# Optimization experiments

Measured on AMD Instinct MI355X. Metric: run time of the kernel, lower is better.

## Reference

```python
import jax, jax.numpy as jnp
import numpy as np
from jax import lax

R, D = 600, 240          # n_rna, n_dis
N = R + D                # graph nodes
H, C = 8, 64             # heads, per-head out channels
E = 20000                # edges
NEG_SLOPE = 0.2
F_CNN = 6 * (64 + 61 + 49 + 33)  # 1242 = concat of four conv branches


def setup_inputs():
    key = jax.random.key(0)
    ks = jax.random.split(key, 25)
    g = lambda i, shape, s=0.1: (jax.random.normal(ks[i], shape, jnp.float32) * s)
    return {
        'edge_index': jax.random.randint(ks[0], (2, E), 0, N, jnp.int32),
        'met_feature': jax.random.normal(ks[1], (R, R), jnp.float32),
        'dis_feature': jax.random.normal(ks[2], (D, D), jnp.float32),
        'rel_matrix': (jax.random.uniform(ks[3], (R, D)) < 0.1).astype(jnp.float32),
        'W_rna': g(4, (R, C)), 'W_dis': g(5, (D, C)),
        'W_l': g(6, (C, H * C)), 'b_l': jnp.zeros((H * C,), jnp.float32),
        'W_r': g(7, (C, H * C)), 'b_r': jnp.zeros((H * C,), jnp.float32),
        'att': g(8, (H, C)), 'gat_bias': jnp.zeros((H * C,), jnp.float32),
        'conv1_w': g(9, (6, 1, H, 1)), 'conv1_b': jnp.zeros((6,), jnp.float32),
        'conv4_w': g(10, (6, 1, H, 4)), 'conv4_b': jnp.zeros((6,), jnp.float32),
        'conv16_w': g(11, (6, 1, H, 16)), 'conv16_b': jnp.zeros((6,), jnp.float32),
        'conv32_w': g(12, (6, 1, H, 32)), 'conv32_b': jnp.zeros((6,), jnp.float32),
        'W_fc': g(13, (F_CNN, F_CNN), 0.02), 'b_fc': jnp.zeros((F_CNN,), jnp.float32),
    }


def gatv2(x, edge_index, W_l, b_l, W_r, b_r, att, bias):
    """GATv2Conv with concat=True and self-loops (eval mode, no dropout)."""
    loop = jnp.arange(N, dtype=edge_index.dtype)
    src = jnp.concatenate([edge_index[0], loop])
    dst = jnp.concatenate([edge_index[1], loop])
    xl = (x @ W_l + b_l).reshape(N, H, C)   # source transform
    xr = (x @ W_r + b_r).reshape(N, H, C)   # target transform
    e = jax.nn.leaky_relu(xl[src] + xr[dst], NEG_SLOPE)      # [Etot,H,C]
    logits = jnp.einsum('ehc,hc->eh', e, att)                 # [Etot,H]
    m = jax.ops.segment_max(logits, dst, num_segments=N)      # [N,H]
    ex = jnp.exp(logits - m[dst])
    denom = jax.ops.segment_sum(ex, dst, num_segments=N)
    alpha = ex / (denom[dst] + 1e-16)                         # edge softmax per dst
    out = jax.ops.segment_sum(alpha[:, :, None] * xl[src], dst, num_segments=N)
    return out.reshape(N, H * C) + bias


def conv_branch(x, w, b):
    # x: [N,1,H,C], w: [6,1,H,k] -> valid conv collapses head dim -> [N,6,1,C-k+1]
    y = lax.conv_general_dilated(x, w, (1, 1), 'VALID',
                                 dimension_numbers=('NCHW', 'OIHW', 'NCHW'))
    y = jax.nn.relu(y + b[None, :, None, None])
    return y.reshape(y.shape[0], -1)


def reference(edge_index, met_feature, dis_feature, rel_matrix, W_rna, W_dis,
              W_l, b_l, W_r, b_r, att, gat_bias,
              conv1_w, conv1_b, conv4_w, conv4_b, conv16_w, conv16_b,
              conv32_w, conv32_b, W_fc, b_fc):
    met_f = met_feature @ W_rna                 # [R,C]
    dis_f = dis_feature @ W_dis                 # [D,C]
    h = jnp.concatenate([met_f, dis_f], axis=0)  # [N,C]
    res = gatv2(h, edge_index, W_l, b_l, W_r, b_r, att, gat_bias)  # [N,H*C]
    x = res.reshape(N, 1, H, C)
    cat = jnp.concatenate([
        conv_branch(x, conv1_w, conv1_b),
        conv_branch(x, conv4_w, conv4_b),
        conv_branch(x, conv16_w, conv16_b),
        conv_branch(x, conv32_w, conv32_b)], axis=1)             # [N,F_CNN]
    feat = jax.nn.relu(cat @ W_fc + b_fc)                        # FeatureTransform
    rna, dis = feat[:R], feat[R:]
    # vectorized replacement of the python double loop: pairwise elementwise product
    pairs = (rna[:, None, :] * dis[None, :, :]).reshape(R * D, F_CNN)
    labels = rel_matrix.reshape(-1, 1)
    return (pairs, labels)
```

## Files before the change

### kernel.cpp

```cpp
#include <hip/hip_runtime.h>
#include <hip/hip_bf16.h>

#define R_ 600
#define D_ 240
#define N_ 840
#define H_ 8
#define C_ 64
#define HC_ 512
#define E_ 20000
#define NE_ 20840
#define F_ 1242
#define PAIRS_ 144000
#define NEG_SLOPE 0.2f

#define OFF_H     0
#define OFF_XL    53760
#define OFF_XR    483840
#define OFF_LOG   913920
#define OFF_MKEY  1080640
#define OFF_DEN   1087360
#define OFF_RES   1094080
#define OFF_CAT   1524160
#define OFF_FEAT  2567440
#define WS_END    3610720
#define ZERO_OFF  OFF_MKEY
#define ZERO_CNT  (6720 + 6720 + 430080)

__device__ __forceinline__ unsigned fkey(float x) {
    unsigned u = __float_as_uint(x);
    return (u & 0x80000000u) ? ~u : (u | 0x80000000u);
}
__device__ __forceinline__ float funkey(unsigned k) {
    unsigned u = (k & 0x80000000u) ? (k ^ 0x80000000u) : ~k;
    return __uint_as_float(u);
}

__global__ void k_zero(float* ws) {
    int i = blockIdx.x * 256 + threadIdx.x;
    if (i < ZERO_CNT) ws[ZERO_OFF + i] = 0.0f;
}

__global__ void k_h(const float* __restrict__ met, const float* __restrict__ dis,
                    const float* __restrict__ Wr,  const float* __restrict__ Wd,
                    float* __restrict__ ws) {
    __shared__ float row_s[R_];
    int n = blockIdx.x, c = threadIdx.x;
    const float *src, *W; int K;
    if (n < R_) { src = met + (size_t)n * R_; W = Wr; K = R_; }
    else        { src = dis + (size_t)(n - R_) * D_; W = Wd; K = D_; }
    for (int k = c; k < K; k += 64) row_s[k] = src[k];
    __syncthreads();
    float acc = 0.f;
    for (int k = 0; k < K; ++k) acc = fmaf(row_s[k], W[k * C_ + c], acc);
    ws[OFF_H + n * C_ + c] = acc;
}

__global__ void k_xlr(const float* __restrict__ Wl, const float* __restrict__ bl,
                      const float* __restrict__ Wr, const float* __restrict__ br,
                      float* __restrict__ ws) {
    __shared__ float hs[C_];
    int n = blockIdx.x, j = threadIdx.x;
    if (j < C_) hs[j] = ws[OFF_H + n * C_ + j];
    __syncthreads();
    float al = bl[j], ar = br[j];
    #pragma unroll
    for (int k = 0; k < C_; ++k) {
        float hv = hs[k];
        al = fmaf(hv, Wl[k * HC_ + j], al);
        ar = fmaf(hv, Wr[k * HC_ + j], ar);
    }
    ws[OFF_XL + n * HC_ + j] = al;
    ws[OFF_XR + n * HC_ + j] = ar;
}

__global__ void k_logits(const int* __restrict__ ei, const float* __restrict__ att,
                         float* __restrict__ ws) {
    int wave = blockIdx.x * 4 + (threadIdx.x >> 6);
    int lane = threadIdx.x & 63;
    if (wave >= NE_) return;
    int e = wave, src, dst;
    if (e < E_) { src = ei[e]; dst = ei[E_ + e]; }
    else        { src = dst = e - E_; }
    const float* xls = ws + OFF_XL + (size_t)src * HC_;
    const float* xrs = ws + OFF_XR + (size_t)dst * HC_;
    unsigned* mkey = (unsigned*)(ws + OFF_MKEY);
    #pragma unroll
    for (int hh = 0; hh < H_; ++hh) {
        float v = xls[hh * C_ + lane] + xrs[hh * C_ + lane];
        v = v > 0.f ? v : NEG_SLOPE * v;
        float p = att[hh * C_ + lane] * v;
        #pragma unroll
        for (int o = 32; o; o >>= 1) p += __shfl_xor(p, o, 64);
        if (lane == 0) {
            ws[OFF_LOG + e * H_ + hh] = p;
            atomicMax(&mkey[dst * H_ + hh], fkey(p));
        }
    }
}

__global__ void k_accum(const int* __restrict__ ei, float* __restrict__ ws) {
    int wave = blockIdx.x * 4 + (threadIdx.x >> 6);
    int lane = threadIdx.x & 63;
    if (wave >= NE_) return;
    int e = wave, src, dst;
    if (e < E_) { src = ei[e]; dst = ei[E_ + e]; }
    else        { src = dst = e - E_; }
    const float* xls = ws + OFF_XL + (size_t)src * HC_;
    const unsigned* mkey = (const unsigned*)(ws + OFF_MKEY);
    float* den = ws + OFF_DEN;
    float* res = ws + OFF_RES + (size_t)dst * HC_;
    #pragma unroll
    for (int hh = 0; hh < H_; ++hh) {
        float lg = ws[OFF_LOG + e * H_ + hh];
        float m  = funkey(mkey[dst * H_ + hh]);
        float ex = expf(lg - m);
        if (lane == 0) atomicAdd(&den[dst * H_ + hh], ex);
        atomicAdd(&res[hh * C_ + lane], ex * xls[hh * C_ + lane]);
    }
}

__global__ void k_conv(const float* __restrict__ gbias,
                       const float* __restrict__ c1w, const float* __restrict__ c1b,
                       const float* __restrict__ c4w, const float* __restrict__ c4b,
                       const float* __restrict__ c16w, const float* __restrict__ c16b,
                       const float* __restrict__ c32w, const float* __restrict__ c32b,
                       float* __restrict__ ws) {
    __shared__ float xsh[HC_];
    __shared__ float wsh[2544];
    __shared__ float cbs[24];
    int n = blockIdx.x, t = threadIdx.x;
    for (int i = t; i < 48;   i += 256) wsh[i]        = c1w[i];
    for (int i = t; i < 192;  i += 256) wsh[48 + i]   = c4w[i];
    for (int i = t; i < 768;  i += 256) wsh[240 + i]  = c16w[i];
    for (int i = t; i < 1536; i += 256) wsh[1008 + i] = c32w[i];
    if (t < 6) { cbs[t] = c1b[t]; cbs[6 + t] = c4b[t]; cbs[12 + t] = c16b[t]; cbs[18 + t] = c32b[t]; }
    for (int i = t; i < HC_; i += 256) {
        int hh = i >> 6;
        float d = ws[OFF_DEN + n * H_ + hh] + 1e-16f;
        xsh[i] = ws[OFF_RES + (size_t)n * HC_ + i] / d + gbias[i];
    }
    __syncthreads();
    for (int f = t; f < F_; f += 256) {
        int k, o, w, wof; float bias;
        if (f < 384)       { k = 1;  o = f / 64;  w = f - o * 64;              wof = 0;    bias = cbs[o]; }
        else if (f < 750)  { k = 4;  int f2 = f - 384;  o = f2 / 61; w = f2 - o * 61; wof = 48;   bias = cbs[6 + o]; }
        else if (f < 1044) { k = 16; int f2 = f - 750;  o = f2 / 49; w = f2 - o * 49; wof = 240;  bias = cbs[12 + o]; }
        else               { k = 32; int f2 = f - 1044; o = f2 / 33; w = f2 - o * 33; wof = 1008; bias = cbs[18 + o]; }
        float acc = bias;
        const float* wp = &wsh[wof + o * H_ * k];
        for (int hh = 0; hh < H_; ++hh)
            for (int dw = 0; dw < k; ++dw)
                acc = fmaf(xsh[hh * C_ + w + dw], wp[hh * k + dw], acc);
        ws[OFF_CAT + (size_t)n * F_ + f] = acc > 0.f ? acc : 0.f;
    }
}

#define BM 64
#define BN 64
#define BK 32
__global__ __launch_bounds__(256) void k_fc(const float* __restrict__ Wfc,
                                            const float* __restrict__ bfc,
                                            float* __restrict__ ws) {
    __shared__ float As[BK][BM + 4];
    __shared__ float Bs[BK][BN];
    const float* A = ws + OFF_CAT;
    float* Cc = ws + OFF_FEAT;
    int bm = blockIdx.y * BM, bn = blockIdx.x * BN;
    int t = threadIdx.x, tx = t & 15, ty = t >> 4;
    float acc[4][4] = {};
    for (int k0 = 0; k0 < F_; k0 += BK) {
        #pragma unroll
        for (int q = 0; q < 8; ++q) {
            int idx = q * 256 + t;
            int ml = idx >> 5, kl = idx & 31;
            int gm = bm + ml, gk = k0 + kl;
            As[kl][ml] = (gm < N_ && gk < F_) ? A[(size_t)gm * F_ + gk] : 0.f;
            int kb = idx >> 6, nb = idx & 63;
            int gkb = k0 + kb, gn = bn + nb;
            Bs[kb][nb] = (gkb < F_ && gn < F_) ? Wfc[(size_t)gkb * F_ + gn] : 0.f;
        }
        __syncthreads();
        #pragma unroll
        for (int kk = 0; kk < BK; ++kk) {
            float a[4], b[4];
            #pragma unroll
            for (int i = 0; i < 4; ++i) a[i] = As[kk][ty * 4 + i];
            #pragma unroll
            for (int j = 0; j < 4; ++j) b[j] = Bs[kk][tx * 4 + j];
            #pragma unroll
            for (int i = 0; i < 4; ++i)
                #pragma unroll
                for (int j = 0; j < 4; ++j)
                    acc[i][j] = fmaf(a[i], b[j], acc[i][j]);
        }
        __syncthreads();
    }
    #pragma unroll
    for (int i = 0; i < 4; ++i) {
        int gm = bm + ty * 4 + i;
        if (gm >= N_) break;
        #pragma unroll
        for (int j = 0; j < 4; ++j) {
            int gn = bn + tx * 4 + j;
            if (gn < F_) {
                float v = acc[i][j] + bfc[gn];
                Cc[(size_t)gm * F_ + gn] = v > 0.f ? v : 0.f;
            }
        }
    }
}

#define PPB 32
__global__ __launch_bounds__(256) void k_pairs(const float* __restrict__ ws, float* __restrict__ out) {
    int t = threadIdx.x;
    for (int pp = 0; pp < PPB; ++pp) {
        int p = blockIdx.x * PPB + pp;
        int i = p / D_, j = p - i * D_;
        const float2* rr = (const float2*)(ws + OFF_FEAT + (size_t)i * F_);
        const float2* dd = (const float2*)(ws + OFF_FEAT + (size_t)(R_ + j) * F_);
        float2* oo = (float2*)(out + (size_t)p * F_);
        for (int x = t; x < F_ / 2; x += 256) {
            float2 a = rr[x], b = dd[x];
            oo[x] = make_float2(a.x * b.x, a.y * b.y);
        }
    }
}

__global__ void k_labels(const float* __restrict__ rel, float* __restrict__ out) {
    int i = blockIdx.x * 256 + threadIdx.x;
    if (i < PAIRS_) out[(size_t)PAIRS_ * F_ + i] = rel[i];
}

extern "C" void kernel_launch(void* const* d_in, const int* in_sizes, int n_in,
                              void* d_out, int out_size, void* d_ws, size_t ws_size,
                              hipStream_t stream) {
    const int*   ei   = (const int*)  d_in[0];
    const float* met  = (const float*)d_in[1];
    const float* dis  = (const float*)d_in[2];
    const float* rel  = (const float*)d_in[3];
    const float* Wrna = (const float*)d_in[4];
    const float* Wdis = (const float*)d_in[5];
    const float* Wl   = (const float*)d_in[6];
    const float* bl   = (const float*)d_in[7];
    const float* Wr   = (const float*)d_in[8];
    const float* br   = (const float*)d_in[9];
    const float* att  = (const float*)d_in[10];
    const float* gb   = (const float*)d_in[11];
    const float* c1w  = (const float*)d_in[12];
    const float* c1b  = (const float*)d_in[13];
    const float* c4w  = (const float*)d_in[14];
    const float* c4b  = (const float*)d_in[15];
    const float* c16w = (const float*)d_in[16];
    const float* c16b = (const float*)d_in[17];
    const float* c32w = (const float*)d_in[18];
    const float* c32b = (const float*)d_in[19];
    const float* Wfc  = (const float*)d_in[20];
    const float* bfc  = (const float*)d_in[21];
    float* ws  = (float*)d_ws;
    float* out = (float*)d_out;

    hipLaunchKernelGGL(k_zero,   dim3((ZERO_CNT + 255) / 256), dim3(256), 0, stream, ws);
    hipLaunchKernelGGL(k_h,      dim3(N_),   dim3(64),  0, stream, met, dis, Wrna, Wdis, ws);
    hipLaunchKernelGGL(k_xlr,    dim3(N_),   dim3(512), 0, stream, Wl, bl, Wr, br, ws);
    hipLaunchKernelGGL(k_logits, dim3((NE_ + 3) / 4), dim3(256), 0, stream, ei, att, ws);
    hipLaunchKernelGGL(k_accum,  dim3((NE_ + 3) / 4), dim3(256), 0, stream, ei, ws);
    hipLaunchKernelGGL(k_conv,   dim3(N_),   dim3(256), 0, stream,
                       gb, c1w, c1b, c4w, c4b, c16w, c16b, c32w, c32b, ws);
    hipLaunchKernelGGL(k_fc,     dim3((F_ + BN - 1) / BN, (N_ + BM - 1) / BM), dim3(256), 0, stream, Wfc, bfc, ws);
    hipLaunchKernelGGL(k_pairs,  dim3(PAIRS_ / PPB), dim3(256), 0, stream, ws, out);
    hipLaunchKernelGGL(k_labels, dim3((PAIRS_ + 255) / 256), dim3(256), 0, stream, rel, out);
}
```

Before: 1.248 ms.

## Replace atomic edge-scatter GATv2 with CSR-by-destination per-node softmax aggregation

Builds a CSR grouping of edges by destination using a histogram, a single-block scan and a scatter. One block per destination node then computes logits, the softmax and the weighted sum without float atomics, and applies normalization and bias before writing. This removes the atomicMax/atomicAdd traffic on the result rows and the logits buffer. The FC GEMM tile height is halved to launch more blocks. It relies on a fixed MAXDEG of 256 shared-memory slots per node, so higher in-degree would overflow, and it adds three small launches.

```diff
diff --git a/kernel.cpp b/kernel.cpp
--- a/kernel.cpp
+++ b/kernel.cpp
@@ -12,32 +12,23 @@
 #define F_ 1242
 #define PAIRS_ 144000
 #define NEG_SLOPE 0.2f
+#define MAXDEG 256
 
 #define OFF_H     0
 #define OFF_XL    53760
 #define OFF_XR    483840
-#define OFF_LOG   913920
-#define OFF_MKEY  1080640
-#define OFF_DEN   1087360
-#define OFF_RES   1094080
-#define OFF_CAT   1524160
-#define OFF_FEAT  2567440
-#define WS_END    3610720
-#define ZERO_OFF  OFF_MKEY
-#define ZERO_CNT  (6720 + 6720 + 430080)
-
-__device__ __forceinline__ unsigned fkey(float x) {
-    unsigned u = __float_as_uint(x);
-    return (u & 0x80000000u) ? ~u : (u | 0x80000000u);
-}
-__device__ __forceinline__ float funkey(unsigned k) {
-    unsigned u = (k & 0x80000000u) ? (k ^ 0x80000000u) : ~k;
-    return __uint_as_float(u);
-}
+#define OFF_RES   913920
+#define OFF_CAT   1344000
+#define OFF_FEAT  2387280
+#define OFF_DEG   3430560
+#define OFF_OFFS  3431400
+#define OFF_POS   3432241
+#define OFF_ESRC  3433081
+#define WS_END    3453921
 
 __global__ void k_zero(float* ws) {
     int i = blockIdx.x * 256 + threadIdx.x;
-    if (i < ZERO_CNT) ws[ZERO_OFF + i] = 0.0f;
+    if (i < N_) ((int*)(ws + OFF_DEG))[i] = 0;
 }
 
 __global__ void k_h(const float* __restrict__ met, const float* __restrict__ dis,
@@ -73,54 +64,100 @@
     ws[OFF_XR + n * HC_ + j] = ar;
 }
 
-__global__ void k_logits(const int* __restrict__ ei, const float* __restrict__ att,
-                         float* __restrict__ ws) {
-    int wave = blockIdx.x * 4 + (threadIdx.x >> 6);
-    int lane = threadIdx.x & 63;
-    if (wave >= NE_) return;
-    int e = wave, src, dst;
+__global__ void k_hist(const int* __restrict__ ei, float* __restrict__ ws) {
+    int e = blockIdx.x * 256 + threadIdx.x;
+    if (e >= NE_) return;
+    int dst = (e < E_) ? ei[E_ + e] : e - E_;
+    atomicAdd((int*)(ws + OFF_DEG) + dst, 1);
+}
+
+__global__ __launch_bounds__(1024) void k_scan(float* __restrict__ ws) {
+    __shared__ int sa[1024], sb[1024];
+    int t = threadIdx.x;
+    const int* deg = (const int*)(ws + OFF_DEG);
+    int* offs = (int*)(ws + OFF_OFFS);
+    int* pos  = (int*)(ws + OFF_POS);
+    int d = (t < N_) ? deg[t] : 0;
+    sa[t] = d;
+    __syncthreads();
+    int *cur = sa, *nxt = sb;
+    for (int off = 1; off < 1024; off <<= 1) {
+        int v = cur[t] + (t >= off ? cur[t - off] : 0);
+        nxt[t] = v;
+        __syncthreads();
+        int* tmp = cur; cur = nxt; nxt = tmp;
+    }
+    if (t < N_) {
+        offs[t + 1] = cur[t];
+        pos[t] = cur[t] - d;
+    }
+    if (t == 0) offs[0] = 0;
+}
+
+__global__ void k_scatter(const int* __restrict__ ei, float* __restrict__ ws) {
+    int e = blockIdx.x * 256 + threadIdx.x;
+    if (e >= NE_) return;
+    int src, dst;
     if (e < E_) { src = ei[e]; dst = ei[E_ + e]; }
     else        { src = dst = e - E_; }
-    const float* xls = ws + OFF_XL + (size_t)src * HC_;
-    const float* xrs = ws + OFF_XR + (size_t)dst * HC_;
-    unsigned* mkey = (unsigned*)(ws + OFF_MKEY);
-    #pragma unroll
-    for (int hh = 0; hh < H_; ++hh) {
-        float v = xls[hh * C_ + lane] + xrs[hh * C_ + lane];
-        v = v > 0.f ? v : NEG_SLOPE * v;
-        float p = att[hh * C_ + lane] * v;
-        #pragma unroll
-        for (int o = 32; o; o >>= 1) p += __shfl_xor(p, o, 64);
-        if (lane == 0) {
-            ws[OFF_LOG + e * H_ + hh] = p;
-            atomicMax(&mkey[dst * H_ + hh], fkey(p));
-        }
-    }
-}
-
-__global__ void k_accum(const int* __restrict__ ei, float* __restrict__ ws) {
-    int wave = blockIdx.x * 4 + (threadIdx.x >> 6);
-    int lane = threadIdx.x & 63;
-    if (wave >= NE_) return;
-    int e = wave, src, dst;
-    if (e < E_) { src = ei[e]; dst = ei[E_ + e]; }
-    else        { src = dst = e - E_; }
-    const float* xls = ws + OFF_XL + (size_t)src * HC_;
-    const unsigned* mkey = (const unsigned*)(ws + OFF_MKEY);
-    float* den = ws + OFF_DEN;
-    float* res = ws + OFF_RES + (size_t)dst * HC_;
-    #pragma unroll
-    for (int hh = 0; hh < H_; ++hh) {
-        float lg = ws[OFF_LOG + e * H_ + hh];
-        float m  = funkey(mkey[dst * H_ + hh]);
-        float ex = expf(lg - m);
-        if (lane == 0) atomicAdd(&den[dst * H_ + hh], ex);
-        atomicAdd(&res[hh * C_ + lane], ex * xls[hh * C_ + lane]);
-    }
-}
-
-__global__ void k_conv(const float* __restrict__ gbias,
-                       const float* __restrict__ c1w, const float* __restrict__ c1b,
+    int idx = atomicAdd((int*)(ws + OFF_POS) + dst, 1);
+    ((int*)(ws + OFF_ESRC))[idx] = src;
+}
+
+__global__ __launch_bounds__(256) void k_gat(const float* __restrict__ att,
+                                             const float* __restrict__ gbias,
+                                             float* __restrict__ ws) {
+    __shared__ int   s_src[MAXDEG];
+    __shared__ float s_w[MAXDEG][H_];
+    __shared__ float s_d[H_];
+    int dst = blockIdx.x, t = threadIdx.x;
+    const int* offs = (const int*)(ws + OFF_OFFS);
+    const int* esrc = (const int*)(ws + OFF_ESRC);
+    int beg = offs[dst], deg = offs[dst + 1] - beg;
+    for (int i = t; i < deg; i += 256) s_src[i] = esrc[beg + i];
+    __syncthreads();
+    int lane = t & 63, g = t >> 6;
+    const float* xr_row = ws + OFF_XR + (size_t)dst * HC_;
+    for (int hh = g; hh < H_; hh += 4) {
+        float a  = att[hh * C_ + lane];
+        float xr = xr_row[hh * C_ + lane];
+        for (int i = 0; i < deg; ++i) {
+            float v = ws[OFF_XL + (size_t)s_src[i] * HC_ + hh * C_ + lane] + xr;
+            v = v > 0.f ? v : NEG_SLOPE * v;
+            float p = a * v;
+            #pragma unroll
+            for (int o = 32; o; o >>= 1) p += __shfl_xor(p, o, 64);
+            if (lane == 0) s_w[i][hh] = p;
+        }
+    }
+    __syncthreads();
+    if (t < 64) {
+        int h = t >> 3, sub = t & 7;
+        float m = -3.4e38f;
+        for (int i = sub; i < deg; i += 8) m = fmaxf(m, s_w[i][h]);
+        #pragma unroll
+        for (int o = 4; o; o >>= 1) m = fmaxf(m, __shfl_xor(m, o, 64));
+        float s = 0.f;
+        for (int i = sub; i < deg; i += 8) {
+            float ex = expf(s_w[i][h] - m);
+            s_w[i][h] = ex;
+            s += ex;
+        }
+        #pragma unroll
+        for (int o = 4; o; o >>= 1) s += __shfl_xor(s, o, 64);
+        if (sub == 0) s_d[h] = s;
+    }
+    __syncthreads();
+    float* out_row = ws + OFF_RES + (size_t)dst * HC_;
+    for (int hh = g; hh < H_; hh += 4) {
+        float acc = 0.f;
+        for (int i = 0; i < deg; ++i)
+            acc = fmaf(s_w[i][hh], ws[OFF_XL + (size_t)s_src[i] * HC_ + hh * C_ + lane], acc);
+        out_row[hh * C_ + lane] = acc / (s_d[hh] + 1e-16f) + gbias[hh * C_ + lane];
+    }
+}
+
+__global__ void k_conv(const float* __restrict__ c1w, const float* __restrict__ c1b,
                        const float* __restrict__ c4w, const float* __restrict__ c4b,
                        const float* __restrict__ c16w, const float* __restrict__ c16b,
                        const float* __restrict__ c32w, const float* __restrict__ c32b,
@@ -134,11 +171,7 @@
     for (int i = t; i < 768;  i += 256) wsh[240 + i]  = c16w[i];
     for (int i = t; i < 1536; i += 256) wsh[1008 + i] = c32w[i];
     if (t < 6) { cbs[t] = c1b[t]; cbs[6 + t] = c4b[t]; cbs[12 + t] = c16b[t]; cbs[18 + t] = c32b[t]; }
-    for (int i = t; i < HC_; i += 256) {
-        int hh = i >> 6;
-        float d = ws[OFF_DEN + n * H_ + hh] + 1e-16f;
-        xsh[i] = ws[OFF_RES + (size_t)n * HC_ + i] / d + gbias[i];
-    }
+    for (int i = t; i < HC_; i += 256) xsh[i] = ws[OFF_RES + (size_t)n * HC_ + i];
     __syncthreads();
     for (int f = t; f < F_; f += 256) {
         int k, o, w, wof; float bias;
@@ -155,26 +188,30 @@
     }
 }
 
-#define BM 64
+#define BM 32
 #define BN 64
 #define BK 32
 __global__ __launch_bounds__(256) void k_fc(const float* __restrict__ Wfc,
                                             const float* __restrict__ bfc,
                                             float* __restrict__ ws) {
-    __shared__ float As[BK][BM + 4];
+    __shared__ float As[BK][BM + 2];
     __shared__ float Bs[BK][BN];
     const float* A = ws + OFF_CAT;
     float* Cc = ws + OFF_FEAT;
     int bm = blockIdx.y * BM, bn = blockIdx.x * BN;
     int t = threadIdx.x, tx = t & 15, ty = t >> 4;
-    float acc[4][4] = {};
+    float acc[2][4] = {};
     for (int k0 = 0; k0 < F_; k0 += BK) {
         #pragma unroll
-        for (int q = 0; q < 8; ++q) {
+        for (int q = 0; q < 4; ++q) {
             int idx = q * 256 + t;
             int ml = idx >> 5, kl = idx & 31;
             int gm = bm + ml, gk = k0 + kl;
             As[kl][ml] = (gm < N_ && gk < F_) ? A[(size_t)gm * F_ + gk] : 0.f;
+        }
+        #pragma unroll
+        for (int q = 0; q < 8; ++q) {
+            int idx = q * 256 + t;
             int kb = idx >> 6, nb = idx & 63;
             int gkb = k0 + kb, gn = bn + nb;
             Bs[kb][nb] = (gkb < F_ && gn < F_) ? Wfc[(size_t)gkb * F_ + gn] : 0.f;
@@ -182,13 +219,13 @@
         __syncthreads();
         #pragma unroll
         for (int kk = 0; kk < BK; ++kk) {
-            float a[4], b[4];
+            float a[2], b[4];
             #pragma unroll
-            for (int i = 0; i < 4; ++i) a[i] = As[kk][ty * 4 + i];
+            for (int i = 0; i < 2; ++i) a[i] = As[kk][ty * 2 + i];
             #pragma unroll
             for (int j = 0; j < 4; ++j) b[j] = Bs[kk][tx * 4 + j];
             #pragma unroll
-            for (int i = 0; i < 4; ++i)
+            for (int i = 0; i < 2; ++i)
                 #pragma unroll
                 for (int j = 0; j < 4; ++j)
                     acc[i][j] = fmaf(a[i], b[j], acc[i][j]);
@@ -196,8 +233,8 @@
         __syncthreads();
     }
     #pragma unroll
-    for (int i = 0; i < 4; ++i) {
-        int gm = bm + ty * 4 + i;
+    for (int i = 0; i < 2; ++i) {
+        int gm = bm + ty * 2 + i;
         if (gm >= N_) break;
         #pragma unroll
         for (int j = 0; j < 4; ++j) {
@@ -259,14 +296,16 @@
     float* ws  = (float*)d_ws;
     float* out = (float*)d_out;
 
-    hipLaunchKernelGGL(k_zero,   dim3((ZERO_CNT + 255) / 256), dim3(256), 0, stream, ws);
-    hipLaunchKernelGGL(k_h,      dim3(N_),   dim3(64),  0, stream, met, dis, Wrna, Wdis, ws);
-    hipLaunchKernelGGL(k_xlr,    dim3(N_),   dim3(512), 0, stream, Wl, bl, Wr, br, ws);
-    hipLaunchKernelGGL(k_logits, dim3((NE_ + 3) / 4), dim3(256), 0, stream, ei, att, ws);
-    hipLaunchKernelGGL(k_accum,  dim3((NE_ + 3) / 4), dim3(256), 0, stream, ei, ws);
-    hipLaunchKernelGGL(k_conv,   dim3(N_),   dim3(256), 0, stream,
-                       gb, c1w, c1b, c4w, c4b, c16w, c16b, c32w, c32b, ws);
-    hipLaunchKernelGGL(k_fc,     dim3((F_ + BN - 1) / BN, (N_ + BM - 1) / BM), dim3(256), 0, stream, Wfc, bfc, ws);
-    hipLaunchKernelGGL(k_pairs,  dim3(PAIRS_ / PPB), dim3(256), 0, stream, ws, out);
-    hipLaunchKernelGGL(k_labels, dim3((PAIRS_ + 255) / 256), dim3(256), 0, stream, rel, out);
-}
+    hipLaunchKernelGGL(k_zero,    dim3(4),    dim3(256), 0, stream, ws);
+    hipLaunchKernelGGL(k_h,       dim3(N_),   dim3(64),  0, stream, met, dis, Wrna, Wdis, ws);
+    hipLaunchKernelGGL(k_xlr,     dim3(N_),   dim3(512), 0, stream, Wl, bl, Wr, br, ws);
+    hipLaunchKernelGGL(k_hist,    dim3((NE_ + 255) / 256), dim3(256), 0, stream, ei, ws);
+    hipLaunchKernelGGL(k_scan,    dim3(1),    dim3(1024), 0, stream, ws);
+    hipLaunchKernelGGL(k_scatter, dim3((NE_ + 255) / 256), dim3(256), 0, stream, ei, ws);
+    hipLaunchKernelGGL(k_gat,     dim3(N_),   dim3(256), 0, stream, att, gb, ws);
+    hipLaunchKernelGGL(k_conv,    dim3(N_),   dim3(256), 0, stream,
+                       c1w, c1b, c4w, c4b, c16w, c16b, c32w, c32b, ws);
+    hipLaunchKernelGGL(k_fc,      dim3((F_ + BN - 1) / BN, (N_ + BM - 1) / BM), dim3(256), 0, stream, Wfc, bfc, ws);
+    hipLaunchKernelGGL(k_pairs,   dim3(PAIRS_ / PPB), dim3(256), 0, stream, ws, out);
+    hipLaunchKernelGGL(k_labels,  dim3((PAIRS_ + 255) / 256), dim3(256), 0, stream, rel, out);
+}
```

New measurement: 1.220 ms. -2.2%, faster.
